# Optimization experiments

Measured on AMD Instinct MI355X. Metric: run time of the kernel, lower is better.

## Reference

```python
import jax, jax.numpy as jnp
import numpy as np

D_CONV = 4
D_STATE = 16
DT_RANK = 64


def _silu(x):
    return x * jax.nn.sigmoid(x)


def setup_inputs() -> dict:
    key = jax.random.key(0)
    ks = jax.random.split(key, 10)
    B, L, dim = 2, 1024, 1024
    d_inner = 2 * dim
    s = lambda fan: 1.0 / np.sqrt(fan)
    inp = {
        "x": jax.random.normal(ks[0], (B, L, dim), jnp.float32),
        "ln_w": jnp.ones((dim,), jnp.float32),
        "ln_b": jnp.zeros((dim,), jnp.float32),
        "w_in": jax.random.normal(ks[1], (2 * d_inner, dim), jnp.float32) * s(dim),
        "conv_w": jax.random.normal(ks[2], (d_inner, D_CONV), jnp.float32) * s(D_CONV),
        "conv_b": jnp.zeros((d_inner,), jnp.float32),
        "w_xproj": jax.random.normal(ks[3], (DT_RANK + 2 * D_STATE, d_inner), jnp.float32) * s(d_inner),
        "w_dt": jax.random.normal(ks[4], (d_inner, DT_RANK), jnp.float32) * s(DT_RANK),
        "b_dt": jax.random.normal(ks[5], (d_inner,), jnp.float32) * 0.1,
        # S4D-real init: A = -(1..d_state) per channel
        "a_log": jnp.tile(jnp.log(jnp.arange(1, D_STATE + 1, dtype=jnp.float32)), (d_inner, 1)),
        "d_skip": jnp.ones((d_inner,), jnp.float32),
        "w_out": jax.random.normal(ks[6], (dim, d_inner), jnp.float32) * s(d_inner),
    }
    return inp


def reference(x, ln_w, ln_b, w_in, conv_w, conv_b, w_xproj, w_dt, b_dt, a_log, d_skip, w_out):
    B, L, dim = x.shape
    residual = x

    # LayerNorm
    mu = jnp.mean(x, axis=-1, keepdims=True)
    var = jnp.mean((x - mu) ** 2, axis=-1, keepdims=True)
    xn = (x - mu) * jax.lax.rsqrt(var + 1e-5) * ln_w + ln_b

    # in_proj -> (x_ssm, z) each (B, L, d_inner)
    xz = jnp.einsum("bld,ed->ble", xn, w_in)
    d_inner = xz.shape[-1] // 2
    xs, z = xz[..., :d_inner], xz[..., d_inner:]

    # depthwise causal conv1d (kernel D_CONV) + SiLU
    xp = jnp.pad(xs, ((0, 0), (D_CONV - 1, 0), (0, 0)))
    xc = conv_b
    for k in range(D_CONV):
        xc = xc + conv_w[:, k] * xp[:, k : k + L, :]
    u = _silu(xc)  # (B, L, d_inner)

    # x_proj -> dt, B, C
    x_dbl = jnp.einsum("ble,re->blr", u, w_xproj)
    dt_r = x_dbl[..., :DT_RANK]
    B_ssm = x_dbl[..., DT_RANK : DT_RANK + D_STATE]         # (B, L, n)
    C_ssm = x_dbl[..., DT_RANK + D_STATE :]                 # (B, L, n)

    dt = jax.nn.softplus(jnp.einsum("blr,er->ble", dt_r, w_dt) + b_dt)  # (B, L, d_inner)

    A = -jnp.exp(a_log)  # (d_inner, n)
    deltaA = jnp.exp(jnp.einsum("ble,en->blen", dt, A))            # (B, L, e, n)
    deltaBu = jnp.einsum("ble,bln,ble->blen", dt, B_ssm, u)        # (B, L, e, n)

    # selective scan over L
    def step(h, ins):
        dA_t, dBu_t, C_t = ins
        h = dA_t * h + dBu_t                       # (B, e, n)
        y = jnp.einsum("ben,bn->be", h, C_t)
        return h, y

    h0 = jnp.zeros((B, d_inner, D_STATE), xs.dtype)
    _, ys = jax.lax.scan(
        step,
        h0,
        (deltaA.transpose(1, 0, 2, 3), deltaBu.transpose(1, 0, 2, 3), C_ssm.transpose(1, 0, 2)),
    )
    y = ys.transpose(1, 0, 2) + u * d_skip         # (B, L, e)

    y = y * _silu(z)
    out = jnp.einsum("ble,de->bld", y, w_out)
    return residual + out
```

## Files before the change

### kernel.cpp

```cpp
#include <hip/hip_runtime.h>
#include <hip/hip_bf16.h>


#define LC 32
#define NCHUNK 32

typedef short bf16x8 __attribute__((ext_vector_type(8)));
typedef float f32x4  __attribute__((ext_vector_type(4)));

static __device__ __forceinline__ float siluf(float x) { return x / (1.f + __expf(-x)); }
static __device__ __forceinline__ unsigned short f2bf(float f) {
    unsigned int u = __float_as_uint(f);
    unsigned int r = (u + 0x7fffu + ((u >> 16) & 1u)) >> 16;
    return (unsigned short)r;
}
static __device__ __forceinline__ float bfb(unsigned short u) {
    return __uint_as_float(((unsigned int)u) << 16);
}
static __device__ __forceinline__ void gload_lds16(const void* g, void* l) {
    __builtin_amdgcn_global_load_lds(
        (const __attribute__((address_space(1))) void*)g,
        (__attribute__((address_space(3))) void*)l, 16, 0, 0);
}

__global__ __launch_bounds__(256) void setup_kernel(
    const float* __restrict__ w_in,  unsigned short* __restrict__ w_in_b,
    const float* __restrict__ w_out, unsigned short* __restrict__ w_out_b,
    const float* __restrict__ w_dt,  unsigned short* __restrict__ w_dt_b,
    const float* __restrict__ x,
    const float* __restrict__ ln_w,
    const float* __restrict__ ln_b,
    unsigned short* __restrict__ xn)
{
    int bid = blockIdx.x, tid = threadIdx.x;
    if (bid < 6272) {
        int i = bid * 256 + tid;
        const float* in; unsigned short* outp; int j;
        if (i < 1048576)      { in = w_in;  outp = w_in_b;  j = i; }
        else if (i < 1572864) { in = w_out; outp = w_out_b; j = i - 1048576; }
        else if (i < 1605632) { in = w_dt;  outp = w_dt_b;  j = i - 1572864; }
        else return;
        float4 v = reinterpret_cast<const float4*>(in)[j];
        ushort4 o = { f2bf(v.x), f2bf(v.y), f2bf(v.z), f2bf(v.w) };
        reinterpret_cast<ushort4*>(outp)[j] = o;
        return;
    }
    int m = bid - 6272;
    const float4* xr = reinterpret_cast<const float4*>(x) + (size_t)m * 256;
    float4 r = xr[tid];
    float f0 = r.x, f1 = r.y, f2 = r.z, f3 = r.w;
    float s  = f0 + f1 + f2 + f3;
    float s2 = f0*f0 + f1*f1 + f2*f2 + f3*f3;
    #pragma unroll
    for (int off = 32; off > 0; off >>= 1) {
        s  += __shfl_down(s, off);
        s2 += __shfl_down(s2, off);
    }
    __shared__ float red[8];
    if ((tid & 63) == 0) { red[tid >> 6] = s; red[4 + (tid >> 6)] = s2; }
    __syncthreads();
    float st = red[0] + red[1] + red[2] + red[3];
    float qt = red[4] + red[5] + red[6] + red[7];
    float mu   = st * (1.f / 1024.f);
    float var  = qt * (1.f / 1024.f) - mu * mu;
    float rstd = rsqrtf(var + 1e-5f);
    float4 wv = reinterpret_cast<const float4*>(ln_w)[tid];
    float4 bv = reinterpret_cast<const float4*>(ln_b)[tid];
    ushort4 o = { f2bf((f0 - mu) * rstd * wv.x + bv.x),
                  f2bf((f1 - mu) * rstd * wv.y + bv.y),
                  f2bf((f2 - mu) * rstd * wv.z + bv.z),
                  f2bf((f3 - mu) * rstd * wv.w + bv.w) };
    reinterpret_cast<ushort4*>(xn + (size_t)m * 1024)[tid] = o;
}

__global__ __launch_bounds__(256) void gemm_bf16_nt(
    const unsigned short* __restrict__ A, int lda,
    const unsigned short* __restrict__ B, int ldb,
    int Kslice,
    float* __restrict__ C, unsigned short* __restrict__ Cb, int ldc,
    const float* __restrict__ bias,
    int ep, size_t Cstride)
{
    __shared__ short As[3 * 64 * 32];
    __shared__ short Bs[3 * 128 * 32];
    int tid = threadIdx.x;
    int z = blockIdx.z;
    A += (size_t)z * Kslice;
    B += (size_t)z * Kslice;
    C += (size_t)z * Cstride;
    int m0 = blockIdx.y * 64, n0 = blockIdx.x * 128;
    int lane = tid & 63, wave = tid >> 6;
    int wm = (wave >> 1) * 32, wn = (wave & 1) * 64;
    int frow = lane & 15, fq = lane >> 4;

    f32x4 acc[2][4] = {};

    int lrow = lane >> 2;
    int scol = (lane & 3) * 8;
    const unsigned short* AgL = A + (size_t)(m0 + wave * 16 + lrow) * lda + scol;
    const unsigned short* BgL = B + (size_t)(n0 + wave * 16 + lrow) * ldb + scol;
    int aoff = (wave * 16) * 32;
    int boff = (wave * 16) * 32;

    #pragma unroll
    for (int p = 0; p < 2; ++p) {
        int nk = p * 32;
        gload_lds16(AgL + nk,                    As + p * 2048 + aoff);
        gload_lds16(BgL + nk,                    Bs + p * 4096 + boff);
        gload_lds16(BgL + (size_t)64 * ldb + nk, Bs + p * 4096 + boff + 64 * 32);
    }

    int cur = 0;
    for (int k0 = 0; k0 < Kslice; k0 += 32) {
        if (k0 + 32 < Kslice) {
            asm volatile("s_waitcnt vmcnt(3) lgkmcnt(0)" ::: "memory");
        } else {
            asm volatile("s_waitcnt vmcnt(0) lgkmcnt(0)" ::: "memory");
        }
        __builtin_amdgcn_s_barrier();
        int nk = k0 + 64;
        if (nk < Kslice) {
            int stg = cur - 1; if (stg < 0) stg = 2;
            gload_lds16(AgL + nk,                    As + stg * 2048 + aoff);
            gload_lds16(BgL + nk,                    Bs + stg * 4096 + boff);
            gload_lds16(BgL + (size_t)64 * ldb + nk, Bs + stg * 4096 + boff + 64 * 32);
        }
        const short* Ac = As + cur * 2048;
        const short* Bc = Bs + cur * 4096;
        bf16x8 af[2], bfr[4];
        #pragma unroll
        for (int i = 0; i < 2; ++i)
            af[i] = *reinterpret_cast<const bf16x8*>(Ac + (wm + i * 16 + frow) * 32 + fq * 8);
        #pragma unroll
        for (int j = 0; j < 4; ++j)
            bfr[j] = *reinterpret_cast<const bf16x8*>(Bc + (wn + j * 16 + frow) * 32 + fq * 8);
        #pragma unroll
        for (int i = 0; i < 2; ++i)
            #pragma unroll
            for (int j = 0; j < 4; ++j)
                acc[i][j] = __builtin_amdgcn_mfma_f32_16x16x32_bf16(af[i], bfr[j], acc[i][j], 0, 0, 0);
        cur = (cur == 2) ? 0 : cur + 1;
    }

    int cn = lane & 15, rq = (lane >> 4) * 4;
    #pragma unroll
    for (int i = 0; i < 2; ++i) {
        #pragma unroll
        for (int j = 0; j < 4; ++j) {
            #pragma unroll
            for (int r = 0; r < 4; ++r) {
                int row = m0 + wm + i * 16 + rq + r;
                int col = n0 + wn + j * 16 + cn;
                float v = acc[i][j][r];
                if (ep == 0) {
                    C[(size_t)row * ldc + col] = v;
                } else if (ep == 1) {
                    v += bias[col];
                    v = (v > 20.f) ? v : log1pf(__expf(v));
                    Cb[(size_t)row * ldc + col] = f2bf(v);
                } else {
                    Cb[(size_t)row * ldc + col] = f2bf(v);
                }
            }
        }
    }
}

__global__ __launch_bounds__(256) void out_reduce(
    const float* __restrict__ part, const float* __restrict__ x,
    float* __restrict__ out)
{
    int i = blockIdx.x * 256 + threadIdx.x;
    float4 s = reinterpret_cast<const float4*>(x)[i];
    #pragma unroll
    for (int z = 0; z < 4; ++z) {
        float4 p = reinterpret_cast<const float4*>(part + (size_t)z * 2097152)[i];
        s.x += p.x; s.y += p.y; s.z += p.z; s.w += p.w;
    }
    reinterpret_cast<float4*>(out)[i] = s;
}

__global__ __launch_bounds__(256) void xproj_splitk(
    const unsigned short* __restrict__ A,
    const float* __restrict__ B,
    float* __restrict__ part)
{
    __shared__ float As[16][68];
    __shared__ float Bs[16][100];
    int tid = threadIdx.x;
    int m0 = blockIdx.x * 64;
    int k0 = blockIdx.y * 128;
    int tx = tid & 15;
    int ty = tid >> 4;
    float acc[4][6] = {};
    int arow = tid >> 2, akg = (tid & 3) << 2;
    int brow1 = (256 + tid) >> 2, bkg1 = ((256 + tid) & 3) << 2;

    for (int ks = 0; ks < 128; ks += 16) {
        ushort4 au = *reinterpret_cast<const ushort4*>(A + (size_t)(m0 + arow) * 2048 + k0 + ks + akg);
        float4 av = make_float4(bfb(au.x), bfb(au.y), bfb(au.z), bfb(au.w));
        float4 bv0 = make_float4(0.f, 0.f, 0.f, 0.f), bv1 = bv0;
        if (arow < 96)  bv0 = *reinterpret_cast<const float4*>(B + (size_t)arow * 2048 + k0 + ks + akg);
        if (brow1 < 96) bv1 = *reinterpret_cast<const float4*>(B + (size_t)brow1 * 2048 + k0 + ks + bkg1);
        __syncthreads();
        As[akg + 0][arow] = av.x; As[akg + 1][arow] = av.y;
        As[akg + 2][arow] = av.z; As[akg + 3][arow] = av.w;
        if (arow < 96) {
            Bs[akg + 0][arow] = bv0.x; Bs[akg + 1][arow] = bv0.y;
            Bs[akg + 2][arow] = bv0.z; Bs[akg + 3][arow] = bv0.w;
        }
        if (brow1 < 96) {
            Bs[bkg1 + 0][brow1] = bv1.x; Bs[bkg1 + 1][brow1] = bv1.y;
            Bs[bkg1 + 2][brow1] = bv1.z; Bs[bkg1 + 3][brow1] = bv1.w;
        }
        __syncthreads();
        #pragma unroll
        for (int k = 0; k < 16; ++k) {
            float aa[4], bb[6];
            #pragma unroll
            for (int i = 0; i < 4; ++i) aa[i] = As[k][ty * 4 + i];
            #pragma unroll
            for (int j = 0; j < 6; ++j) bb[j] = Bs[k][tx * 6 + j];
            #pragma unroll
            for (int i = 0; i < 4; ++i)
                #pragma unroll
                for (int j = 0; j < 6; ++j)
                    acc[i][j] = fmaf(aa[i], bb[j], acc[i][j]);
        }
    }
    float* p = part + (size_t)blockIdx.y * 196608;
    #pragma unroll
    for (int i = 0; i < 4; ++i)
        #pragma unroll
        for (int j = 0; j < 6; ++j)
            p[(size_t)(m0 + ty * 4 + i) * 96 + tx * 6 + j] = acc[i][j];
}

__global__ __launch_bounds__(256) void xproj_reduce(
    const float* __restrict__ part, float* __restrict__ xdbl,
    unsigned short* __restrict__ dtr)
{
    int i = blockIdx.x * 256 + threadIdx.x;
    float s = 0.f;
    #pragma unroll
    for (int sd = 0; sd < 16; ++sd) s += part[(size_t)sd * 196608 + i];
    xdbl[i] = s;
    int m = i / 96, col = i - m * 96;
    if (col < 64) dtr[(size_t)m * 64 + col] = f2bf(s);
}

__global__ __launch_bounds__(256) void conv_silu_kernel(
    const unsigned short* __restrict__ xz,
    const float* __restrict__ cw,
    const float* __restrict__ cb,
    unsigned short* __restrict__ u)
{
    int idx = blockIdx.x * 256 + threadIdx.x;
    int e = idx & 2047;
    int mp = idx >> 11;
    int m0 = mp * 2;
    int l0 = m0 & 1023;
    float r[5];
    #pragma unroll
    for (int k = 0; k < 5; ++k) {
        int lr = l0 - 3 + k;
        r[k] = (lr >= 0) ? bfb(xz[(size_t)(m0 - 3 + k) * 4096 + e]) : 0.f;
    }
    float4 w = *reinterpret_cast<const float4*>(cw + e * 4);
    float base = cb[e];
    float a0 = base + w.x * r[0] + w.y * r[1] + w.z * r[2] + w.w * r[3];
    float a1 = base + w.x * r[1] + w.y * r[2] + w.z * r[3] + w.w * r[4];
    u[(size_t)m0 * 2048 + e]       = f2bf(siluf(a0));
    u[(size_t)(m0 + 1) * 2048 + e] = f2bf(siluf(a1));
}

__global__ __launch_bounds__(256) void scan_part1(
    const unsigned short* __restrict__ dt,
    const unsigned short* __restrict__ u,
    const float* __restrict__ xdbl,
    const float* __restrict__ a_log,
    float* __restrict__ hpart,
    float* __restrict__ Aprod)
{
    int tid = threadIdx.x;
    int ch = tid >> 2, ng = tid & 3;
    int bid = blockIdx.x;
    int c = bid & 31, et = (bid >> 5) & 31, b = bid >> 10;
    int e = et * 64 + ch;
    float4 al = *reinterpret_cast<const float4*>(a_log + e * 16 + ng * 4);
    float A0 = -__expf(al.x), A1 = -__expf(al.y), A2 = -__expf(al.z), A3 = -__expf(al.w);
    size_t rbase = (size_t)b * 1024 + c * LC;
    const unsigned short* dt_p = dt + rbase * 2048 + e;
    const unsigned short* u_p  = u  + rbase * 2048 + e;
    const float* b_p  = xdbl + rbase * 96 + 64 + ng * 4;
    float h0 = 0.f, h1 = 0.f, h2 = 0.f, h3 = 0.f;
    float P0 = 1.f, P1 = 1.f, P2 = 1.f, P3 = 1.f;
    float dt_c = bfb(dt_p[0]);
    float u_c  = bfb(u_p[0]);
    float4 B_c = *reinterpret_cast<const float4*>(b_p);
    #pragma unroll 8
    for (int l = 0; l < LC; ++l) {
        float dt_n = bfb(dt_p[(size_t)(l + 1) * 2048]);
        float u_n  = bfb(u_p[(size_t)(l + 1) * 2048]);
        float4 B_n = *reinterpret_cast<const float4*>(b_p + (size_t)(l + 1) * 96);
        float du = dt_c * u_c;
        float d0 = __expf(dt_c * A0), d1 = __expf(dt_c * A1);
        float d2 = __expf(dt_c * A2), d3 = __expf(dt_c * A3);
        h0 = fmaf(d0, h0, du * B_c.x); P0 *= d0;
        h1 = fmaf(d1, h1, du * B_c.y); P1 *= d1;
        h2 = fmaf(d2, h2, du * B_c.z); P2 *= d2;
        h3 = fmaf(d3, h3, du * B_c.w); P3 *= d3;
        dt_c = dt_n; u_c = u_n; B_c = B_n;
    }
    size_t oidx = (size_t)c * 65536 + ((size_t)b * 2048 + e) * 16 + ng * 4;
    *reinterpret_cast<float4*>(hpart + oidx) = make_float4(h0, h1, h2, h3);
    *reinterpret_cast<float4*>(Aprod + oidx) = make_float4(P0, P1, P2, P3);
}

__global__ __launch_bounds__(256) void scan_combine(
    const float* __restrict__ hpart,
    const float* __restrict__ Aprod,
    float* __restrict__ hinit)
{
    int t = blockIdx.x * 256 + threadIdx.x;
    float h = 0.f;
    #pragma unroll 8
    for (int c = 0; c < NCHUNK; ++c) {
        hinit[(size_t)c * 65536 + t] = h;
        float P  = Aprod[(size_t)c * 65536 + t];
        float hp = hpart[(size_t)c * 65536 + t];
        h = fmaf(P, h, hp);
    }
}

__global__ __launch_bounds__(256) void scan_part2(
    const unsigned short* __restrict__ dt,
    const unsigned short* __restrict__ u,
    const float* __restrict__ xdbl,
    const unsigned short* __restrict__ xz,
    const float* __restrict__ a_log,
    const float* __restrict__ d_skip,
    const float* __restrict__ hinit,
    unsigned short* __restrict__ y)
{
    int tid = threadIdx.x;
    int ch = tid >> 2, ng = tid & 3;
    int bid = blockIdx.x;
    int c = bid & 31, et = (bid >> 5) & 31, b = bid >> 10;
    int e = et * 64 + ch;
    float4 al = *reinterpret_cast<const float4*>(a_log + e * 16 + ng * 4);
    float A0 = -__expf(al.x), A1 = -__expf(al.y), A2 = -__expf(al.z), A3 = -__expf(al.w);
    float dsk = d_skip[e];
    size_t rbase = (size_t)b * 1024 + c * LC;
    const unsigned short* dt_p = dt + rbase * 2048 + e;
    const unsigned short* u_p  = u  + rbase * 2048 + e;
    const unsigned short* z_p  = xz + rbase * 4096 + 2048 + e;
    const float* bc_p = xdbl + rbase * 96 + 64 + ng * 4;
    unsigned short* y_p = y + rbase * 2048 + e;
    size_t oidx = (size_t)c * 65536 + ((size_t)b * 2048 + e) * 16 + ng * 4;
    float4 hi = *reinterpret_cast<const float4*>(hinit + oidx);
    float h0 = hi.x, h1 = hi.y, h2 = hi.z, h3 = hi.w;
    float dt_c = bfb(dt_p[0]);
    float u_c  = bfb(u_p[0]);
    float4 B_c = *reinterpret_cast<const float4*>(bc_p);
    float4 C_c = *reinterpret_cast<const float4*>(bc_p + 16);
    #pragma unroll 8
    for (int l = 0; l < LC; ++l) {
        float dt_n = bfb(dt_p[(size_t)(l + 1) * 2048]);
        float u_n  = bfb(u_p[(size_t)(l + 1) * 2048]);
        float4 B_n = *reinterpret_cast<const float4*>(bc_p + (size_t)(l + 1) * 96);
        float4 C_n = *reinterpret_cast<const float4*>(bc_p + (size_t)(l + 1) * 96 + 16);
        float du = dt_c * u_c;
        float d0 = __expf(dt_c * A0), d1 = __expf(dt_c * A1);
        float d2 = __expf(dt_c * A2), d3 = __expf(dt_c * A3);
        h0 = fmaf(d0, h0, du * B_c.x);
        h1 = fmaf(d1, h1, du * B_c.y);
        h2 = fmaf(d2, h2, du * B_c.z);
        h3 = fmaf(d3, h3, du * B_c.w);
        float p = h0 * C_c.x + h1 * C_c.y + h2 * C_c.z + h3 * C_c.w;
        p += __shfl_xor(p, 1);
        p += __shfl_xor(p, 2);
        if (ng == 0) {
            float zv = bfb(z_p[(size_t)l * 4096]);
            y_p[(size_t)l * 2048] = f2bf((p + u_c * dsk) * siluf(zv));
        }
        dt_c = dt_n; u_c = u_n; B_c = B_n; C_c = C_n;
    }
}

extern "C" void kernel_launch(void* const* d_in, const int* in_sizes, int n_in,
                              void* d_out, int out_size, void* d_ws, size_t ws_size,
                              hipStream_t stream) {
    const float* x       = (const float*)d_in[0];
    const float* ln_w    = (const float*)d_in[1];
    const float* ln_b    = (const float*)d_in[2];
    const float* w_in    = (const float*)d_in[3];
    const float* conv_w  = (const float*)d_in[4];
    const float* conv_b  = (const float*)d_in[5];
    const float* w_xproj = (const float*)d_in[6];
    const float* w_dt    = (const float*)d_in[7];
    const float* b_dt    = (const float*)d_in[8];
    const float* a_log   = (const float*)d_in[9];
    const float* d_skip  = (const float*)d_in[10];
    const float* w_out   = (const float*)d_in[11];
    float* out = (float*)d_out;

    float* ws = (float*)d_ws;
    unsigned short* xn_b    = (unsigned short*)(ws);
    unsigned short* xz_b    = (unsigned short*)(ws + 1048576);
    unsigned short* u_b     = (unsigned short*)(ws + 5242880);
    float* xdbl  = ws + 7340032;
    unsigned short* dt_b    = (unsigned short*)(ws + 7536640);
    float* hpart = ws + 9633792;
    float* Aprod = ws + 13828096;
    float* hinit = ws + 18022400;
    unsigned short* y_b     = (unsigned short*)(ws + 22216704);
    unsigned short* w_in_b  = (unsigned short*)(ws + 24313856);
    unsigned short* w_out_b = (unsigned short*)(ws + 26411008);
    unsigned short* w_dt_b  = (unsigned short*)(ws + 27459584);
    unsigned short* dtr_b   = (unsigned short*)(ws + 27525120);
    float* xpart = ws + 9633792;
    float* opart = ws + 1048576;

    setup_kernel<<<8320, 256, 0, stream>>>(w_in, w_in_b, w_out, w_out_b, w_dt, w_dt_b,
                                           x, ln_w, ln_b, xn_b);
    gemm_bf16_nt<<<dim3(32, 32, 1), 256, 0, stream>>>(xn_b, 1024, w_in_b, 1024, 1024,
                                                      nullptr, xz_b, 4096, nullptr, 3, 0);
    conv_silu_kernel<<<8192, 256, 0, stream>>>(xz_b, conv_w, conv_b, u_b);
    xproj_splitk<<<dim3(32, 16), 256, 0, stream>>>(u_b, w_xproj, xpart);
    xproj_reduce<<<768, 256, 0, stream>>>(xpart, xdbl, dtr_b);
    gemm_bf16_nt<<<dim3(16, 32, 1), 256, 0, stream>>>(dtr_b, 64, w_dt_b, 64, 64,
                                                      nullptr, dt_b, 2048, b_dt, 1, 0);
    scan_part1<<<2048, 256, 0, stream>>>(dt_b, u_b, xdbl, a_log, hpart, Aprod);
    scan_combine<<<256, 256, 0, stream>>>(hpart, Aprod, hinit);
    scan_part2<<<2048, 256, 0, stream>>>(dt_b, u_b, xdbl, xz_b, a_log, d_skip, hinit, y_b);
    gemm_bf16_nt<<<dim3(8, 32, 4), 256, 0, stream>>>(y_b, 2048, w_out_b, 2048, 512,
                                                     opart, nullptr, 1024, nullptr, 0, 2097152);
    out_reduce<<<2048, 256, 0, stream>>>(opart, x, out);
}
```

Before: 272.2 us.

## Fuse causal conv+SiLU into x_proj split-K and swizzle GEMM block order

```diff
diff --git a/kernel.cpp b/kernel.cpp
--- a/kernel.cpp
+++ b/kernel.cpp
@@ -88,7 +88,15 @@
     A += (size_t)z * Kslice;
     B += (size_t)z * Kslice;
     C += (size_t)z * Cstride;
-    int m0 = blockIdx.y * 64, n0 = blockIdx.x * 128;
+
+    int gx = gridDim.x;
+    int wg = blockIdx.y * gx + blockIdx.x;
+    int nwg = gx * gridDim.y;
+    int cpx = nwg >> 3;
+    int swz = (wg & 7) * cpx + (wg >> 3);
+    int bx = swz % gx, by = swz / gx;
+
+    int m0 = by * 64, n0 = bx * 128;
     int lane = tid & 63, wave = tid >> 6;
     int wm = (wave >> 1) * 32, wn = (wave & 1) * 64;
     int frow = lane & 15, fq = lane >> 4;
@@ -181,8 +189,11 @@
 }
 
 __global__ __launch_bounds__(256) void xproj_splitk(
-    const unsigned short* __restrict__ A,
+    const unsigned short* __restrict__ xz,
+    const float* __restrict__ cw,
+    const float* __restrict__ cb,
     const float* __restrict__ B,
+    unsigned short* __restrict__ u,
     float* __restrict__ part)
 {
     __shared__ float As[16][68];
@@ -195,16 +206,42 @@
     float acc[4][6] = {};
     int arow = tid >> 2, akg = (tid & 3) << 2;
     int brow1 = (256 + tid) >> 2, bkg1 = ((256 + tid) & 3) << 2;
+    int m = m0 + arow;
+    int l = m & 1023;
 
     for (int ks = 0; ks < 128; ks += 16) {
-        ushort4 au = *reinterpret_cast<const ushort4*>(A + (size_t)(m0 + arow) * 2048 + k0 + ks + akg);
-        float4 av = make_float4(bfb(au.x), bfb(au.y), bfb(au.z), bfb(au.w));
+        int e0 = k0 + ks + akg;
+        float xv[4][4];
+        #pragma unroll
+        for (int kk = 0; kk < 4; ++kk) {
+            ushort4 t = make_ushort4(0, 0, 0, 0);
+            if (l - 3 + kk >= 0)
+                t = *reinterpret_cast<const ushort4*>(xz + (size_t)(m - 3 + kk) * 4096 + e0);
+            xv[kk][0] = bfb(t.x); xv[kk][1] = bfb(t.y);
+            xv[kk][2] = bfb(t.z); xv[kk][3] = bfb(t.w);
+        }
+        float4 cbv = *reinterpret_cast<const float4*>(cb + e0);
+        float cbs[4] = { cbv.x, cbv.y, cbv.z, cbv.w };
+        float res[4];
+        #pragma unroll
+        for (int j = 0; j < 4; ++j) {
+            float4 w = *reinterpret_cast<const float4*>(cw + (size_t)(e0 + j) * 4);
+            float a = cbs[j];
+            a = fmaf(w.x, xv[0][j], a);
+            a = fmaf(w.y, xv[1][j], a);
+            a = fmaf(w.z, xv[2][j], a);
+            a = fmaf(w.w, xv[3][j], a);
+            res[j] = siluf(a);
+        }
+        ushort4 uo = { f2bf(res[0]), f2bf(res[1]), f2bf(res[2]), f2bf(res[3]) };
+        *reinterpret_cast<ushort4*>(u + (size_t)m * 2048 + e0) = uo;
+
         float4 bv0 = make_float4(0.f, 0.f, 0.f, 0.f), bv1 = bv0;
         if (arow < 96)  bv0 = *reinterpret_cast<const float4*>(B + (size_t)arow * 2048 + k0 + ks + akg);
         if (brow1 < 96) bv1 = *reinterpret_cast<const float4*>(B + (size_t)brow1 * 2048 + k0 + ks + bkg1);
         __syncthreads();
-        As[akg + 0][arow] = av.x; As[akg + 1][arow] = av.y;
-        As[akg + 2][arow] = av.z; As[akg + 3][arow] = av.w;
+        As[akg + 0][arow] = res[0]; As[akg + 1][arow] = res[1];
+        As[akg + 2][arow] = res[2]; As[akg + 3][arow] = res[3];
         if (arow < 96) {
             Bs[akg + 0][arow] = bv0.x; Bs[akg + 1][arow] = bv0.y;
             Bs[akg + 2][arow] = bv0.z; Bs[akg + 3][arow] = bv0.w;
@@ -247,31 +284,6 @@
     xdbl[i] = s;
     int m = i / 96, col = i - m * 96;
     if (col < 64) dtr[(size_t)m * 64 + col] = f2bf(s);
-}
-
-__global__ __launch_bounds__(256) void conv_silu_kernel(
-    const unsigned short* __restrict__ xz,
-    const float* __restrict__ cw,
-    const float* __restrict__ cb,
-    unsigned short* __restrict__ u)
-{
-    int idx = blockIdx.x * 256 + threadIdx.x;
-    int e = idx & 2047;
-    int mp = idx >> 11;
-    int m0 = mp * 2;
-    int l0 = m0 & 1023;
-    float r[5];
-    #pragma unroll
-    for (int k = 0; k < 5; ++k) {
-        int lr = l0 - 3 + k;
-        r[k] = (lr >= 0) ? bfb(xz[(size_t)(m0 - 3 + k) * 4096 + e]) : 0.f;
-    }
-    float4 w = *reinterpret_cast<const float4*>(cw + e * 4);
-    float base = cb[e];
-    float a0 = base + w.x * r[0] + w.y * r[1] + w.z * r[2] + w.w * r[3];
-    float a1 = base + w.x * r[1] + w.y * r[2] + w.z * r[3] + w.w * r[4];
-    u[(size_t)m0 * 2048 + e]       = f2bf(siluf(a0));
-    u[(size_t)(m0 + 1) * 2048 + e] = f2bf(siluf(a1));
 }
 
 __global__ __launch_bounds__(256) void scan_part1(
@@ -426,8 +438,8 @@
                                            x, ln_w, ln_b, xn_b);
     gemm_bf16_nt<<<dim3(32, 32, 1), 256, 0, stream>>>(xn_b, 1024, w_in_b, 1024, 1024,
                                                       nullptr, xz_b, 4096, nullptr, 3, 0);
-    conv_silu_kernel<<<8192, 256, 0, stream>>>(xz_b, conv_w, conv_b, u_b);
-    xproj_splitk<<<dim3(32, 16), 256, 0, stream>>>(u_b, w_xproj, xpart);
+    xproj_splitk<<<dim3(32, 16), 256, 0, stream>>>(xz_b, conv_w, conv_b, w_xproj,
+                                                   u_b, xpart);
     xproj_reduce<<<768, 256, 0, stream>>>(xpart, xdbl, dtr_b);
     gemm_bf16_nt<<<dim3(16, 32, 1), 256, 0, stream>>>(dtr_b, 64, w_dt_b, 64, 64,
                                                       nullptr, dt_b, 2048, b_dt, 1, 0);
```

Measured after the change: 267.3 us. Within noise of the previous version (-1.8%).
